# Performance work log

Hardware: AMD Instinct MI355X
Metric: run time of the kernel (lower is better)

The kernel has to match this reference:

```python
import jax, jax.numpy as jnp
import numpy as np
from jax import lax

K = 100
NUM_CLASSES = 80
MIN_X = 1; MIN_Y = 1; MAX_X = 4; MAX_Y = 4   # int(base_layer_range/16) for [16,64,16,64]
KEEP = 300
IOU_TH = 0.5
ROI_H = 2 * MAX_Y + 1  # 9
ROI_W = 2 * MAX_X + 1  # 9
MASK_OUT = 36          # 9 -> two stride-2 deconvs -> 36
SCALE = (36.0 - 1.0) / (9.0 - 1.0)
BN_INV = 1.0 / np.sqrt(1.0 + 1e-3)  # BN eval, running mean 0 / var 1, eps=1e-3
SIZES = [(64, 64), (32, 32), (16, 16)]


def bilinear(img, xx, yy):
    # img [..., H, W]; xx, yy same shape S; border-clamped bilinear sample -> [..., *S]
    H, W = img.shape[-2], img.shape[-1]
    xx = jnp.clip(xx, 0.0, W - 1.0)
    yy = jnp.clip(yy, 0.0, H - 1.0)
    x0f = jnp.floor(xx); y0f = jnp.floor(yy)
    wx = xx - x0f; wy = yy - y0f
    x0 = x0f.astype(jnp.int32); y0 = y0f.astype(jnp.int32)
    x1 = jnp.minimum(x0 + 1, W - 1); y1 = jnp.minimum(y0 + 1, H - 1)
    v00 = img[..., y0, x0]; v01 = img[..., y0, x1]
    v10 = img[..., y1, x0]; v11 = img[..., y1, x1]
    return (1 - wy) * ((1 - wx) * v00 + wx * v01) + wy * ((1 - wx) * v10 + wx * v11)


def roi_align(feat, boxes):
    # feat [C,H,W], boxes [N,4] in feat coords -> [N,C,ROI_H,ROI_W] (sampling_ratio=1)
    n = boxes.shape[0]
    x1, y1, x2, y2 = boxes[:, 0], boxes[:, 1], boxes[:, 2], boxes[:, 3]
    jx = (jnp.arange(ROI_W, dtype=jnp.float32) + 0.5) / ROI_W
    jy = (jnp.arange(ROI_H, dtype=jnp.float32) + 0.5) / ROI_H
    gx = x1[:, None] + (x2 - x1)[:, None] * jx  # [N,ROI_W]
    gy = y1[:, None] + (y2 - y1)[:, None] * jy  # [N,ROI_H]
    xx = jnp.broadcast_to(gx[:, None, :], (n, ROI_H, ROI_W))
    yy = jnp.broadcast_to(gy[:, :, None], (n, ROI_H, ROI_W))
    out = bilinear(feat, xx, yy)  # [C,N,ROI_H,ROI_W]
    return jnp.transpose(out, (1, 0, 2, 3))


def crop_resize(masks, boxes):
    # masks [N,h,w], boxes [N,4] -> [N,MASK_OUT,MASK_OUT]
    n = boxes.shape[0]
    t = jnp.arange(MASK_OUT, dtype=jnp.float32) / (MASK_OUT - 1.0)
    x1, y1, x2, y2 = boxes[:, 0], boxes[:, 1], boxes[:, 2], boxes[:, 3]
    gx = x1[:, None] + (x2 - x1)[:, None] * t
    gy = y1[:, None] + (y2 - y1)[:, None] * t
    xx = jnp.broadcast_to(gx[:, None, :], (n, MASK_OUT, MASK_OUT))
    yy = jnp.broadcast_to(gy[:, :, None], (n, MASK_OUT, MASK_OUT))
    return jax.vmap(bilinear)(masks, xx, yy)


def nms_keep(boxes, scores):
    # greedy NMS, faithful to torchvision semantics; returns bool keep flags [N]
    n = boxes.shape[0]
    x1, y1, x2, y2 = boxes[:, 0], boxes[:, 1], boxes[:, 2], boxes[:, 3]
    area = (x2 - x1) * (y2 - y1)
    ix1 = jnp.maximum(x1[:, None], x1[None, :]); iy1 = jnp.maximum(y1[:, None], y1[None, :])
    ix2 = jnp.minimum(x2[:, None], x2[None, :]); iy2 = jnp.minimum(y2[:, None], y2[None, :])
    inter = jnp.clip(ix2 - ix1, 0.0) * jnp.clip(iy2 - iy1, 0.0)
    iou = inter / (area[:, None] + area[None, :] - inter + 1e-9)
    order = jnp.argsort(-scores)  # stable
    def step(carry, idx):
        supp, keep = carry
        k = jnp.logical_not(supp[idx])
        keep = keep.at[idx].set(k)
        supp = jnp.logical_or(supp, jnp.logical_and(k, iou[idx] > IOU_TH))
        return (supp, keep), None
    init = (jnp.zeros((n,), bool), jnp.zeros((n,), bool))
    (_, keep), _ = lax.scan(step, init, order)
    return keep


def _conv(x, w, b, pad):
    y = lax.conv_general_dilated(x, w, (1, 1), [(pad, pad), (pad, pad)],
                                 dimension_numbers=('NCHW', 'OIHW', 'NCHW'))
    return y + b[None, :, None, None]


def _deconv(x, w, b):
    # ConvTranspose2d(k=2, s=2): fractionally-strided conv, doubles spatial size
    y = lax.conv_general_dilated(x, w, (1, 1), [(1, 1), (1, 1)], lhs_dilation=(2, 2),
                                 dimension_numbers=('NCHW', 'OIHW', 'NCHW'))
    return y + b[None, :, None, None]


def _bn(x, g, b):
    return x * (g * BN_INV)[None, :, None, None] + b[None, :, None, None]


def mask_head(x, c1_w, c1_b, mid_w, mid_b, bn_g, bn_b, d1_w, d1_b, d2_w, d2_b, c5_w, c5_b, c6_w, c6_b):
    r = jax.nn.relu
    h = r(_bn(_conv(x, c1_w, c1_b, 1), bn_g[0], bn_b[0]))
    for j in range(3):  # conv2..conv4
        h = r(_bn(_conv(h, mid_w[j], mid_b[j], 1), bn_g[1 + j], bn_b[1 + j]))
    h = r(_deconv(h, d1_w, d1_b))
    h = r(_bn(_conv(h, c5_w, c5_b, 1), bn_g[4], bn_b[4]))
    h = r(_deconv(h, d2_w, d2_b))
    return jax.nn.sigmoid(_conv(h, c6_w, c6_b, 0))


def _decode_layer(heat, tlr, brr, i, H0, W0):
    C, H, W = heat.shape
    hw = H * W
    scores, inds = lax.top_k(heat.reshape(-1), K)
    clses = (inds // hw).astype(jnp.float32)
    rem = inds % hw
    ys = (rem // W).astype(jnp.float32)
    xs = (rem % W).astype(jnp.float32)
    t = tlr.reshape(2, hw)[:, rem]  # [2,K]
    b = brr.reshape(2, hw)[:, rem]
    rx = float(MAX_X - MIN_X); ry = float(MAX_Y - MIN_Y)
    cx = (MAX_X + MIN_X) / 2.0;  cy = (MAX_Y + MIN_Y) / 2.0
    tlx = jnp.clip(xs - (rx * t[0] + cx), 0.0, float(W))
    tly = jnp.clip(ys - (ry * t[1] + cy), 0.0, float(H))
    brx = jnp.clip(xs + (rx * b[0] + cx), 0.0, float(W))
    bry = jnp.clip(ys + (ry * b[1] + cy), 0.0, float(H))
    boxes = jnp.stack([tlx, tly, brx, bry], 1)
    sc = jnp.where((brx < tlx) | (bry < tly), -1.0, scores)
    mb = jnp.stack([xs - MAX_X, ys - MAX_Y, xs + MAX_X, ys + MAX_Y,
                    jnp.full((K,), float(i))], 1)
    s2, order = lax.top_k(sc, K)  # num_dets(1000) >= K -> full sort by score
    boxes = boxes[order]; mb = mb[order]; cls = clses[order]
    lay = jnp.full((K,), float(i))
    cols = jnp.stack([s2, s2, lay, cls], 1)
    bws = jnp.concatenate([boxes, cols], 1)  # boxes_without_scaling [K,8]
    scale = jnp.array([W0 / W, H0 / H, W0 / W, H0 / H], jnp.float32)
    dets = jnp.concatenate([boxes * scale, cols], 1)
    return dets, bws, mb


def _decode_one(h0, h1, h2, t0, t1, t2, b0, b1, b2, f0, f1, f2,
                c1_w, c1_b, mid_w, mid_b, bn_g, bn_b, d1_w, d1_b, d2_w, d2_b,
                c5_w, c5_b, c6_w, c6_b):
    heats = (h0, h1, h2); tls = (t0, t1, t2); brs = (b0, b1, b2); feats = (f0, f1, f2)
    H0, W0 = heats[0].shape[1], heats[0].shape[2]
    dets_l, bws_l, mb_l = [], [], []
    for i in range(3):
        d, bw, mb = _decode_layer(heats[i], tls[i], brs[i], i, H0, W0)
        dets_l.append(d); bws_l.append(bw); mb_l.append(mb)
    dets = jnp.concatenate(dets_l, 0)   # [300,8]
    bws = jnp.concatenate(bws_l, 0)
    mb = jnp.concatenate(mb_l, 0)       # [300,5]
    # NMS faithful to source: boxes = detections[:,1:5], scores = detections[:,4]
    keep = nms_keep(dets[:, 1:5], dets[:, 4])
    sel = jnp.argsort(-jnp.where(keep, dets[:, 4], -1e9))[:KEEP]
    dets = dets[sel]; bws = bws[sel]; mb = mb[sel]
    # sort by mask layer index descending (features processed last->first)
    ord2 = jnp.argsort(-mb[:, 4])
    dets = dets[ord2]; bws = bws[ord2]; mb = mb[ord2]
    # ROI pool each box from its own layer's feature map
    pooled = jnp.stack([roi_align(feats[i], mb[:, :4]) for i in range(3)], 0)  # [3,N,C,9,9]
    lay = jnp.clip(mb[:, 4].astype(jnp.int32), 0, 2)
    rois = pooled[lay, jnp.arange(KEEP)]  # [N,256,9,9]
    masks_all = mask_head(rois, c1_w, c1_b, mid_w, mid_b, bn_g, bn_b,
                          d1_w, d1_b, d2_w, d2_b, c5_w, c5_b, c6_w, c6_b)  # [N,80,36,36]
    cls = jnp.clip(dets[:, 7].astype(jnp.int32), 0, NUM_CLASSES - 1)
    masks = masks_all[jnp.arange(KEEP), cls]  # [N,36,36] (one-hot scatter/select)
    bws4 = bws[:, :4] - jnp.tile(mb[:, :2], (1, 2))
    norm_boxes = SCALE * bws4
    masks = crop_resize(masks, norm_boxes)
    return dets, masks


def setup_inputs():
    key = jax.random.key(0)
    ks = jax.random.split(key, 32)
    B = 1
    inp = {}
    for i, (H, W) in enumerate(SIZES):
        inp['heat%d' % i] = jax.random.uniform(ks[i], (B, NUM_CLASSES, H, W), jnp.float32)
        inp['tl%d' % i] = 0.1 * jax.random.normal(ks[3 + i], (B, 2, H, W), jnp.float32)
        inp['br%d' % i] = 0.1 * jax.random.normal(ks[6 + i], (B, 2, H, W), jnp.float32)
        inp['feat%d' % i] = jax.random.normal(ks[9 + i], (B, 256, H, W), jnp.float32)
    inp['c1_w'] = 0.05 * jax.random.normal(ks[12], (256, 256, 3, 3), jnp.float32)
    inp['c1_b'] = jnp.zeros((256,), jnp.float32)
    inp['mid_w'] = 0.05 * jax.random.normal(ks[13], (3, 256, 256, 3, 3), jnp.float32)
    inp['mid_b'] = jnp.zeros((3, 256), jnp.float32)
    inp['bn_g'] = jnp.ones((5, 256), jnp.float32)
    inp['bn_b'] = jnp.zeros((5, 256), jnp.float32)
    inp['d1_w'] = 0.05 * jax.random.normal(ks[14], (256, 256, 2, 2), jnp.float32)
    inp['d1_b'] = jnp.zeros((256,), jnp.float32)
    inp['d2_w'] = 0.05 * jax.random.normal(ks[15], (256, 256, 2, 2), jnp.float32)
    inp['d2_b'] = jnp.zeros((256,), jnp.float32)
    inp['c5_w'] = 0.05 * jax.random.normal(ks[16], (256, 256, 3, 3), jnp.float32)
    inp['c5_b'] = jnp.zeros((256,), jnp.float32)
    inp['c6_w'] = 0.05 * jax.random.normal(ks[17], (NUM_CLASSES, 256, 1, 1), jnp.float32)
    inp['c6_b'] = jnp.zeros((NUM_CLASSES,), jnp.float32)
    return inp


def reference(heat0, heat1, heat2, tl0, tl1, tl2, br0, br1, br2, feat0, feat1, feat2,
              c1_w, c1_b, mid_w, mid_b, bn_g, bn_b, d1_w, d1_b, d2_w, d2_b,
              c5_w, c5_b, c6_w, c6_b):
    dets, masks = jax.vmap(_decode_one, in_axes=(0,) * 12 + (None,) * 14)(
        heat0, heat1, heat2, tl0, tl1, tl2, br0, br1, br2, feat0, feat1, feat2,
        c1_w, c1_b, mid_w, mid_b, bn_g, bn_b, d1_w, d1_b, d2_w, d2_b, c5_w, c5_b, c6_w, c6_b)
    return dets, masks  # [B,300,8], [B,300,36,36]
```

## Files before the change

### kernel.cpp

```cpp
#include <hip/hip_runtime.h>
#include <math.h>

typedef __attribute__((ext_vector_type(8))) short bf16x8;
typedef __attribute__((ext_vector_type(4))) float f32x4;

__device__ __forceinline__ unsigned fkey_u(float v){
  unsigned b = __float_as_uint(v);
  return (b & 0x80000000u) ? ~b : (b | 0x80000000u);
}
__device__ __forceinline__ float fkey_inv(unsigned m){
  unsigned b = (m & 0x80000000u) ? (m & 0x7fffffffu) : ~m;
  return __uint_as_float(b);
}
__device__ __forceinline__ unsigned short f2bf(float f){
  unsigned u = __float_as_uint(f);
  unsigned r = (u + 0x7fffu + ((u>>16)&1u)) >> 16;
  return (unsigned short)r;
}
__device__ __forceinline__ unsigned long long shfl_xor_u64(unsigned long long v, int mask){
  int lo = __shfl_xor((int)(unsigned)(v & 0xFFFFFFFFull), mask, 64);
  int hi = __shfl_xor((int)(unsigned)(v >> 32), mask, 64);
  return ((unsigned long long)(unsigned)hi << 32) | (unsigned long long)(unsigned)lo;
}
__device__ __forceinline__ unsigned long long bshfl_u64(unsigned long long v, int lane){
  int lo = __shfl((int)(unsigned)(v & 0xFFFFFFFFull), lane, 64);
  int hi = __shfl((int)(unsigned)(v >> 32), lane, 64);
  return ((unsigned long long)(unsigned)hi << 32) | (unsigned long long)(unsigned)lo;
}
#define BNI 0.9995003746877732f

template<int E, int J>
__device__ __forceinline__ void reg_step(unsigned long long* key, int t, int k2){
  #pragma unroll
  for (int r=0;r<E;r++){
    if ((r & J)==0){
      int e = t*E + r;
      bool desc = ((e & k2)==0);
      unsigned long long a=key[r], b=key[r^J];
      if (desc ? (a<b) : (a>b)){ key[r]=b; key[r^J]=a; }
    }
  }
}
template<int E>
__device__ __forceinline__ void reg_tail(unsigned long long* key, int t, int k2, int jstart){
  if constexpr (E>=8) { if (jstart>=4) reg_step<E,4>(key,t,k2); }
  if constexpr (E>=4) { if (jstart>=2) reg_step<E,2>(key,t,k2); }
  if (jstart>=1) reg_step<E,1>(key,t,k2);
}
template<int E>
__device__ void bitonic_desc(unsigned long long* key, unsigned long long* lds){
  const int t = threadIdx.x;
  const int N = E*256;
  for (int k2=2;k2<=N;k2<<=1){
    for (int j=k2>>1; j>=E; j>>=1){
      int w = j/E;
      bool lower = ((t & w)==0);
      bool desc  = (((t*E) & k2)==0);
      bool keep_max = (desc == lower);
      if (w < 64){
        #pragma unroll
        for (int r=0;r<E;r++){
          unsigned long long mine=key[r];
          unsigned long long o=shfl_xor_u64(mine, w);
          bool gt = mine > o;
          key[r] = keep_max ? (gt?mine:o) : (gt?o:mine);
        }
      } else {
        __syncthreads();
        #pragma unroll
        for (int r=0;r<E;r++) lds[t*E+r]=key[r];
        __syncthreads();
        #pragma unroll
        for (int r=0;r<E;r++){
          unsigned long long mine=key[r];
          unsigned long long o=lds[(t*E+r)^j];
          bool gt = mine > o;
          key[r] = keep_max ? (gt?mine:o) : (gt?o:mine);
        }
      }
    }
    int jstart = ((k2>>1) < (E>>1)) ? (k2>>1) : (E>>1);
    reg_tail<E>(key,t,k2,jstart);
  }
  __syncthreads();
  #pragma unroll
  for (int r=0;r<E;r++) lds[t*E+r]=key[r];
  __syncthreads();
}

__global__ __launch_bounds__(256) void k_sel1(
    const float* __restrict__ h0, const float* __restrict__ h1, const float* __restrict__ h2,
    unsigned long long* __restrict__ c1)
{
  int b = blockIdx.x;
  int layer, chunk;
  if (b < 320){ layer=0; chunk=b; }
  else if (b < 400){ layer=1; chunk=b-320; }
  else { layer=2; chunk=b-400; }
  const float* heat = (layer==0)?h0:((layer==1)?h1:h2);
  __shared__ unsigned long long lds[1024];
  unsigned long long key[4];
  int t = threadIdx.x;
  int base = chunk*1024 + t*4;
  float4 v = *(const float4*)(heat + base);
  key[0] = ((unsigned long long)fkey_u(v.x)<<32) | (unsigned long long)(0xFFFFFFFFu - (unsigned)(base+0));
  key[1] = ((unsigned long long)fkey_u(v.y)<<32) | (unsigned long long)(0xFFFFFFFFu - (unsigned)(base+1));
  key[2] = ((unsigned long long)fkey_u(v.z)<<32) | (unsigned long long)(0xFFFFFFFFu - (unsigned)(base+2));
  key[3] = ((unsigned long long)fkey_u(v.w)<<32) | (unsigned long long)(0xFFFFFFFFu - (unsigned)(base+3));
  bitonic_desc<4>(key, lds);
  if (t<100) c1[(size_t)b*100 + t] = lds[t];
}

__global__ __launch_bounds__(256) void k_sel2(
    const unsigned long long* __restrict__ c1, unsigned long long* __restrict__ c2)
{
  int b = blockIdx.x;
  __shared__ unsigned long long lds[2048];
  unsigned long long key[8];
  int t=threadIdx.x;
  const unsigned long long* src = c1 + (size_t)b*2000;
  #pragma unroll
  for (int r=0;r<8;r++){
    int i=t*8+r;
    key[r] = (i<2000)? src[i] : 0ull;
  }
  bitonic_desc<8>(key, lds);
  if (t<100) c2[(size_t)b*100+t]=lds[t];
}

__global__ __launch_bounds__(256) void k_sel3_decode(
    const unsigned long long* __restrict__ c2,
    const float* __restrict__ tl0,const float* __restrict__ tl1,const float* __restrict__ tl2,
    const float* __restrict__ br0,const float* __restrict__ br1,const float* __restrict__ br2,
    float* __restrict__ dets, float* __restrict__ bws, float* __restrict__ mbw)
{
  int layer = blockIdx.x;
  int hw = 4096 >> (layer*2);
  int W = 64>>layer;
  float Wf = (float)W;
  const float* tl = (layer==0)?tl0:((layer==1)?tl1:tl2);
  const float* br = (layer==0)?br0:((layer==1)?br1:br2);
  int base = (layer==0)?0:((layer==1)?1600:2000);
  int cnt  = (layer==0)?1600:((layer==1)?400:100);
  __shared__ unsigned long long lds[2048];
  __shared__ float scl[100];
  unsigned long long key[8];
  int t = threadIdx.x;
  #pragma unroll
  for (int r=0;r<8;r++){
    int i=t*8+r;
    key[r] = (i<cnt)? c2[base+i] : 0ull;
  }
  bitonic_desc<8>(key, lds);
  unsigned long long kwin=0;
  if (t<100) kwin = lds[t];
  float tlx=0,tly=0,brx=0,bry=0,xs=0,ys=0,clsfv=0,scv=0;
  if (t<100){
    unsigned m=(unsigned)(kwin>>32);
    unsigned gidx = 0xFFFFFFFFu - (unsigned)(kwin & 0xFFFFFFFFull);
    float val = fkey_inv(m);
    int cls = (int)(gidx / (unsigned)hw);
    int rem = (int)(gidx % (unsigned)hw);
    int iy = rem / W, ix = rem % W;
    xs = (float)ix; ys = (float)iy; clsfv = (float)cls;
    float t0=tl[rem], t1=tl[hw+rem], b0=br[rem], b1=br[hw+rem];
    tlx = fminf(fmaxf(xs - (3.0f*t0 + 2.5f), 0.0f), Wf);
    tly = fminf(fmaxf(ys - (3.0f*t1 + 2.5f), 0.0f), Wf);
    brx = fminf(fmaxf(xs + (3.0f*b0 + 2.5f), 0.0f), Wf);
    bry = fminf(fmaxf(ys + (3.0f*b1 + 2.5f), 0.0f), Wf);
    scv = ((brx<tlx)||(bry<tly)) ? -1.0f : val;
    scl[t]=scv;
  }
  __syncthreads();
  if (t<100){
    int rank=0;
    for (int i=0;i<100;i++){
      float si=scl[i];
      rank += ((si>scv)||(si==scv && i<t)) ? 1 : 0;
    }
    int row = layer*100 + rank;
    float sx = (float)(1<<layer);
    float* dr = dets + row*8;
    dr[0]=tlx*sx; dr[1]=tly*sx; dr[2]=brx*sx; dr[3]=bry*sx;
    dr[4]=scv; dr[5]=scv; dr[6]=(float)layer; dr[7]=clsfv;
    float* bwr = bws + row*8;
    bwr[0]=tlx;bwr[1]=tly;bwr[2]=brx;bwr[3]=bry;bwr[4]=scv;bwr[5]=scv;bwr[6]=(float)layer;bwr[7]=clsfv;
    float* mr = mbw + row*5;
    mr[0]=xs-4.0f; mr[1]=ys-4.0f; mr[2]=xs+4.0f; mr[3]=ys+4.0f; mr[4]=(float)layer;
  }
}

#define NMS_STEP(P, OC, M) { \
  int idx=__shfl((OC),(P),64); \
  unsigned long long supw=bshfl_u64(sup, idx>>6); \
  int kq=(int)((~(supw>>(idx&63)))&1ull); \
  if (t==0) keep_[idx]=kq; \
  unsigned long long v0=bshfl_u64(M[0],(P)); \
  unsigned long long v1=bshfl_u64(M[1],(P)); \
  unsigned long long v2=bshfl_u64(M[2],(P)); \
  unsigned long long v3=bshfl_u64(M[3],(P)); \
  unsigned long long v4=bshfl_u64(M[4],(P)); \
  unsigned long long mv=(t==0)?v0:((t==1)?v1:((t==2)?v2:((t==3)?v3:((t==4)?v4:0ull)))); \
  if (kq) sup|=mv; }

__global__ __launch_bounds__(320) void k_nms(
    const float* __restrict__ dets, const float* __restrict__ bws, const float* __restrict__ mbw,
    float* __restrict__ out_dets, float* __restrict__ mbf, int* __restrict__ clsf,
    int* __restrict__ layf, float* __restrict__ nbox)
{
  __shared__ __align__(16) float4 bq[300];
  __shared__ __align__(16) float sc[300];
  __shared__ __align__(16) float kk[300];
  __shared__ __align__(16) float lq[300];
  __shared__ float lyv[300];
  __shared__ unsigned long long sm_ord[300][5];
  __shared__ int order_[300], keep_[300], sel_[300], fperm[300];
  int t = threadIdx.x;
  float X1=0,Y1=0,X2=0,Y2=0,S=0,A=0;
  if (t<300){
    const float* r = dets + t*8;
    X1=r[1];Y1=r[2];X2=r[3];Y2=r[4];
    S=r[4];
    A=(X2-X1)*(Y2-Y1);
    bq[t]=make_float4(X1,Y1,X2,Y2);
    sc[t]=S;
    lyv[t]=mbw[t*5+4];
  }
  __syncthreads();
  if (t<300){
    int rank=0;
    for (int j4=0;j4<75;j4++){
      float4 s4=*(const float4*)&sc[j4*4];
      int j=j4*4;
      rank += ((s4.x>S)||(s4.x==S&&(j+0)<t)) ? 1:0;
      rank += ((s4.y>S)||(s4.y==S&&(j+1)<t)) ? 1:0;
      rank += ((s4.z>S)||(s4.z==S&&(j+2)<t)) ? 1:0;
      rank += ((s4.w>S)||(s4.w==S&&(j+3)<t)) ? 1:0;
    }
    unsigned long long wrow[5];
    #pragma unroll
    for (int jw=0;jw<5;jw++){
      unsigned long long bits=0;
      int lim=(jw==4)?44:64;
      for (int jj=0;jj<lim;jj++){
        int j=jw*64+jj;
        float4 q=bq[j];
        float aj=(q.z-q.x)*(q.w-q.y);
        float ix1=fmaxf(X1,q.x), iy1=fmaxf(Y1,q.y);
        float ix2=fminf(X2,q.z), iy2=fminf(Y2,q.w);
        float it=fmaxf(ix2-ix1,0.f)*fmaxf(iy2-iy1,0.f);
        float iou=it/(A+aj-it+1e-9f);
        bits |= ((unsigned long long)(iou>0.5f))<<jj;
      }
      wrow[jw]=bits;
    }
    order_[rank]=t;
    #pragma unroll
    for (int q=0;q<5;q++) sm_ord[rank][q]=wrow[q];
  }
  __syncthreads();
  if (t<64){
    int o0=order_[t], o1=order_[64+t], o2=order_[128+t], o3=order_[192+t];
    int o4=(t<44)? order_[256+t] : 0;
    unsigned long long m0[5],m1[5],m2[5],m3[5],m4[5];
    #pragma unroll
    for (int q=0;q<5;q++){
      m0[q]=sm_ord[t][q]; m1[q]=sm_ord[64+t][q];
      m2[q]=sm_ord[128+t][q]; m3[q]=sm_ord[192+t][q];
      m4[q]=(t<44)? sm_ord[256+t][q] : 0ull;
    }
    unsigned long long sup=0;
    for (int p=0;p<64;p++) NMS_STEP(p,o0,m0);
    for (int p=0;p<64;p++) NMS_STEP(p,o1,m1);
    for (int p=0;p<64;p++) NMS_STEP(p,o2,m2);
    for (int p=0;p<64;p++) NMS_STEP(p,o3,m3);
    for (int p=0;p<44;p++) NMS_STEP(p,o4,m4);
  }
  __syncthreads();
  if (t<300) kk[t] = keep_[t] ? sc[t] : -1000000000.0f;
  __syncthreads();
  float KV=0; int rank2=0;
  if (t<300){
    KV=kk[t];
    for (int j4=0;j4<75;j4++){
      float4 s4=*(const float4*)&kk[j4*4];
      int j=j4*4;
      rank2 += ((s4.x>KV)||(s4.x==KV&&(j+0)<t)) ? 1:0;
      rank2 += ((s4.y>KV)||(s4.y==KV&&(j+1)<t)) ? 1:0;
      rank2 += ((s4.z>KV)||(s4.z==KV&&(j+2)<t)) ? 1:0;
      rank2 += ((s4.w>KV)||(s4.w==KV&&(j+3)<t)) ? 1:0;
    }
    sel_[rank2]=t;
  }
  __syncthreads();
  if (t<300) lq[t]=lyv[sel_[t]];
  __syncthreads();
  if (t<300){
    float L=lq[t]; int rank3=0;
    for (int j4=0;j4<75;j4++){
      float4 s4=*(const float4*)&lq[j4*4];
      int j=j4*4;
      rank3 += ((s4.x>L)||(s4.x==L&&(j+0)<t)) ? 1:0;
      rank3 += ((s4.y>L)||(s4.y==L&&(j+1)<t)) ? 1:0;
      rank3 += ((s4.z>L)||(s4.z==L&&(j+2)<t)) ? 1:0;
      rank3 += ((s4.w>L)||(s4.w==L&&(j+3)<t)) ? 1:0;
    }
    fperm[rank3]=sel_[t];
  }
  __syncthreads();
  if (t<300){
    int src=fperm[t];
    const float* dr=dets+src*8;
    #pragma unroll
    for (int c=0;c<8;c++) out_dets[t*8+c]=dr[c];
    const float* mr=mbw+src*5;
    #pragma unroll
    for (int c=0;c<5;c++) mbf[t*5+c]=mr[c];
    int cc=(int)dr[7]; cc = cc<0?0:(cc>79?79:cc); clsf[t]=cc;
    int lv=(int)mr[4]; lv = lv<0?0:(lv>2?2:lv); layf[t]=lv;
    const float* bw=bws+src*8;
    nbox[t*4+0]=4.375f*(bw[0]-mr[0]);
    nbox[t*4+1]=4.375f*(bw[1]-mr[1]);
    nbox[t*4+2]=4.375f*(bw[2]-mr[0]);
    nbox[t*4+3]=4.375f*(bw[3]-mr[1]);
  }
}

__global__ __launch_bounds__(256) void k_roi(
    const float* __restrict__ f0,const float* __restrict__ f1,const float* __restrict__ f2,
    const float* __restrict__ mbf, const int* __restrict__ layf,
    unsigned short* __restrict__ rois, int r0)
{
  int nl = blockIdx.x; int g = r0 + nl;
  __shared__ int ix0[9], ix1[9], iy0[9], iy1[9];
  __shared__ float wx[9], wy[9];
  int lay = layf[g];
  int W = 64>>lay;
  float Wf1 = (float)(W-1);
  const float* feat = (lay==0)?f0:((lay==1)?f1:f2);
  int t=threadIdx.x;
  if (t<9){
    float x1=mbf[g*5+0], x2=mbf[g*5+2];
    float jx = ((float)t + 0.5f)/9.0f;
    float gx = x1 + (x2-x1)*jx;
    float xx = fminf(fmaxf(gx,0.0f), Wf1);
    float x0f = floorf(xx);
    wx[t]=xx-x0f;
    int x0=(int)x0f; ix0[t]=x0; ix1[t]=min(x0+1,W-1);
  } else if (t>=16 && t<25){
    int j=t-16;
    float y1=mbf[g*5+1], y2=mbf[g*5+3];
    float jy=((float)j+0.5f)/9.0f;
    float gy=y1+(y2-y1)*jy;
    float yy=fminf(fmaxf(gy,0.0f),Wf1);
    float y0f=floorf(yy);
    wy[j]=yy-y0f;
    int y0=(int)y0f; iy0[j]=y0; iy1[j]=min(y0+1,W-1);
  }
  __syncthreads();
  int c=t;
  const float* fp = feat + (size_t)c*W*W;
  unsigned short* op = rois + (size_t)nl*81*256;
  for (int p=0;p<81;p++){
    int py=p/9, px=p%9;
    float v00=fp[iy0[py]*W+ix0[px]];
    float v01=fp[iy0[py]*W+ix1[px]];
    float v10=fp[iy1[py]*W+ix0[px]];
    float v11=fp[iy1[py]*W+ix1[px]];
    float wxx=wx[px], wyy=wy[py];
    float v = (1.0f-wyy)*((1.0f-wxx)*v00 + wxx*v01) + wyy*((1.0f-wxx)*v10 + wxx*v11);
    op[(size_t)p*256 + c] = f2bf(v);
  }
}

__global__ __launch_bounds__(64) void k_wprep3(
    const float* __restrict__ c1w, const float* __restrict__ midw, const float* __restrict__ c5w,
    unsigned short* __restrict__ WB)
{
  int b = blockIdx.x, c = blockIdx.y, l = threadIdx.x;
  int t = b>>7;
  const float* src = (c==0)? c1w : (c<=3 ? midw + (size_t)(c-1)*589824 : c5w);
  unsigned short* dst = WB + (size_t)c*589824 + ((size_t)b<<9) + l*8;
  int co = (b&15)*16 + (l&15);
  int cib = ((b>>4)&7)*32 + ((l>>4)<<3);
  #pragma unroll
  for (int j=0;j<8;j++) dst[j] = f2bf(src[((size_t)co*256 + cib + j)*9 + t]);
}
__global__ __launch_bounds__(64) void k_wprep2(
    const float* __restrict__ d1w, const float* __restrict__ d2w,
    unsigned short* __restrict__ WD)
{
  int b = blockIdx.x, c = blockIdx.y, l = threadIdx.x;
  int t = b>>7;
  const float* src = (c==0)? d1w : d2w;
  unsigned short* dst = WD + (size_t)c*262144 + ((size_t)b<<9) + l*8;
  int co = (b&15)*16 + (l&15);
  int cib = ((b>>4)&7)*32 + ((l>>4)<<3);
  #pragma unroll
  for (int j=0;j<8;j++) dst[j] = f2bf(src[((size_t)co*256 + cib + j)*4 + t]);
}

__global__ __launch_bounds__(256,3) void k_mconv9h(
    const unsigned short* __restrict__ Xg, unsigned short* __restrict__ Yg,
    const unsigned short* __restrict__ WBc,
    const float* __restrict__ Bc, const float* __restrict__ Gg, const float* __restrict__ Bn)
{
  __shared__ __align__(16) unsigned short Xp[88*264];
  int tid=threadIdx.x, l=tid&63, w=tid>>6;
  int h=blockIdx.y;
  int rlo = h ? 4 : -1;
  const unsigned short* Xr = Xg + (size_t)blockIdx.x*81*256;
  for (int idx=tid; idx<88*32; idx+=256){
    int pp=idx>>5, k8=idx&31;
    int y=pp/11 + rlo, x=pp%11 - 1;
    uint4 v{0,0,0,0};
    if ((unsigned)y<9u && (unsigned)x<9u) v = *(const uint4*)(Xr + ((y*9+x)<<8) + (k8<<3));
    *(uint4*)&Xp[pp*264 + (k8<<3)] = v;
  }
  __syncthreads();
  int mbase = h*48;
  int pixb[3];
  #pragma unroll
  for (int mt=0;mt<3;mt++){
    int m=mbase+mt*16+(l&15); if(m>80)m=80;
    pixb[mt]=(m/9 - rlo)*11 + (m%9) + 1;
  }
  int kg=(l>>4)<<3;
  f32x4 acc[3][4] = {};
  const unsigned short* wbase = WBc + (size_t)l*8;
  for (int t9=0;t9<9;t9++){
    int toff=(t9/3-1)*11 + (t9%3-1);
    for (int kc=0;kc<8;kc++){
      bf16x8 a[3], b[4];
      #pragma unroll
      for (int mt=0;mt<3;mt++) a[mt] = *(const bf16x8*)&Xp[(pixb[mt]+toff)*264 + (kc<<5) + kg];
      #pragma unroll
      for (int nn=0;nn<4;nn++) b[nn] = *(const bf16x8*)(wbase + ((size_t)(((t9<<3)+kc)*16 + (w<<2)+nn)<<9));
      #pragma unroll
      for (int mt=0;mt<3;mt++){
        #pragma unroll
        for (int nn=0;nn<4;nn++)
          acc[mt][nn] = __builtin_amdgcn_mfma_f32_16x16x32_bf16(a[mt], b[nn], acc[mt][nn], 0,0,0);
      }
    }
  }
  unsigned short* Yr = Yg + (size_t)blockIdx.x*81*256;
  int rb=(l>>4)<<2;
  #pragma unroll
  for (int nn=0;nn<4;nn++){
    int co=(w<<6)+(nn<<4)+(l&15);
    float bc=Bc[co], gm=Gg[co]*BNI, bb=Bn[co];
    #pragma unroll
    for (int mt=0;mt<3;mt++){
      #pragma unroll
      for (int r=0;r<4;r++){
        int m=mbase+mt*16+rb+r;
        if (m<81 || h==0){
          if (m<81){
            float v=fmaxf((acc[mt][nn][r]+bc)*gm+bb, 0.f);
            Yr[m*256+co]=f2bf(v);
          }
        }
      }
    }
  }
}

__global__ __launch_bounds__(256,2) void k_mdeconv1(
    const unsigned short* __restrict__ Xg, unsigned short* __restrict__ Yg,
    const unsigned short* __restrict__ WD1, const float* __restrict__ Bd)
{
  __shared__ __align__(16) unsigned short Xp[81*264];
  int tid=threadIdx.x, l=tid&63, w=tid>>6;
  int tp=blockIdx.y;
  const unsigned short* Xr = Xg + (size_t)blockIdx.x*81*256;
  for (int idx=tid; idx<81*32; idx+=256){
    int pp=idx>>5, k8=idx&31;
    *(uint4*)&Xp[pp*264+(k8<<3)] = *(const uint4*)(Xr + (pp<<8)+(k8<<3));
  }
  __syncthreads();
  int pixb[6];
  #pragma unroll
  for (int mt=0;mt<6;mt++){ int m=mt*16+(l&15); pixb[mt]=(m>80)?80:m; }
  int kg=(l>>4)<<3;
  f32x4 acc[6][4] = {};
  const unsigned short* wbase = WD1 + (size_t)tp*65536 + (size_t)l*8;
  for (int kc=0;kc<8;kc++){
    bf16x8 a[6], b[4];
    #pragma unroll
    for (int mt=0;mt<6;mt++) a[mt] = *(const bf16x8*)&Xp[pixb[mt]*264 + (kc<<5) + kg];
    #pragma unroll
    for (int nn=0;nn<4;nn++) b[nn] = *(const bf16x8*)(wbase + ((size_t)(kc*16 + (w<<2)+nn)<<9));
    #pragma unroll
    for (int mt=0;mt<6;mt++){
      #pragma unroll
      for (int nn=0;nn<4;nn++)
        acc[mt][nn] = __builtin_amdgcn_mfma_f32_16x16x32_bf16(a[mt], b[nn], acc[mt][nn], 0,0,0);
    }
  }
  unsigned short* Yr = Yg + (size_t)blockIdx.x*324*256;
  int ky=tp>>1, kx=tp&1;
  int rb=(l>>4)<<2;
  #pragma unroll
  for (int nn=0;nn<4;nn++){
    int co=(w<<6)+(nn<<4)+(l&15);
    float bd=Bd[co];
    #pragma unroll
    for (int mt=0;mt<6;mt++){
      #pragma unroll
      for (int r=0;r<4;r++){
        int m=mt*16+rb+r;
        if (m<81){
          int iy=m/9, ix=m%9;
          int opx=(2*iy+1-ky)*18 + (2*ix+1-kx);
          Yr[opx*256+co]=f2bf(fmaxf(acc[mt][nn][r]+bd,0.f));
        }
      }
    }
  }
}

__global__ __launch_bounds__(256,2) void k_mconv18(
    const unsigned short* __restrict__ Xg, unsigned short* __restrict__ Yg,
    const unsigned short* __restrict__ WBc,
    const float* __restrict__ Bc, const float* __restrict__ Gg, const float* __restrict__ Bn)
{
  __shared__ __align__(16) unsigned short Xp[160*136];
  int tid=threadIdx.x, l=tid&63, w=tid>>6;
  int rg=blockIdx.y, ch=blockIdx.z;
  const unsigned short* Xr = Xg + (size_t)blockIdx.x*324*256;
  int pixb[7];
  #pragma unroll
  for (int mt=0;mt<7;mt++){ int m=mt*16+(l&15); if(m>107)m=107; pixb[mt]=(m/18)*20+(m%18); }
  int kg=(l>>4)<<3;
  f32x4 acc[7][2] = {};
  const unsigned short* wbase = WBc + (size_t)l*8;
  for (int h=0;h<2;h++){
    __syncthreads();
    for (int idx=tid; idx<160*16; idx+=256){
      int pp=idx>>4, k8=idx&15;
      int py=rg*6-1+pp/20, px=pp%20-1;
      uint4 v{0,0,0,0};
      if ((unsigned)py<18u && (unsigned)px<18u)
        v = *(const uint4*)(Xr + ((py*18+px)<<8) + (h<<7) + (k8<<3));
      *(uint4*)&Xp[pp*136 + (k8<<3)] = v;
    }
    __syncthreads();
    for (int t9=0;t9<9;t9++){
      int toff=(t9/3)*20 + (t9%3);
      for (int kc=0;kc<4;kc++){
        int kcg=(h<<2)+kc;
        bf16x8 a[7], b[2];
        #pragma unroll
        for (int mt=0;mt<7;mt++) a[mt] = *(const bf16x8*)&Xp[(pixb[mt]+toff)*136 + (kc<<5) + kg];
        #pragma unroll
        for (int nn=0;nn<2;nn++) b[nn] = *(const bf16x8*)(wbase + ((size_t)(((t9<<3)+kcg)*16 + (ch<<3)+(w<<1)+nn)<<9));
        #pragma unroll
        for (int mt=0;mt<7;mt++){
          #pragma unroll
          for (int nn=0;nn<2;nn++)
            acc[mt][nn] = __builtin_amdgcn_mfma_f32_16x16x32_bf16(a[mt], b[nn], acc[mt][nn], 0,0,0);
        }
      }
    }
  }
  unsigned short* Yr = Yg + (size_t)blockIdx.x*324*256;
  int rb=(l>>4)<<2;
  #pragma unroll
  for (int nn=0;nn<2;nn++){
    int co=(ch<<7)+(w<<5)+(nn<<4)+(l&15);
    float bc=Bc[co], gm=Gg[co]*BNI, bb=Bn[co];
    #pragma unroll
    for (int mt=0;mt<7;mt++){
      #pragma unroll
      for (int r=0;r<4;r++){
        int m=mt*16+rb+r;
        if (m<108){
          int opx=rg*108+m;
          Yr[opx*256+co]=f2bf(fmaxf((acc[mt][nn][r]+bc)*gm+bb, 0.f));
        }
      }
    }
  }
}

__global__ __launch_bounds__(256,2) void k_mdec2c6(
    const unsigned short* __restrict__ Xg,
    const unsigned short* __restrict__ WD2, const float* __restrict__ Bd,
    const float* __restrict__ W6, const float* __restrict__ B6,
    const int* __restrict__ clsf, float* __restrict__ mask36, int r0)
{
  __shared__ __align__(16) unsigned short Xp[108*264];
  __shared__ float part[4][112];
  int tid=threadIdx.x, l=tid&63, w=tid>>6;
  int tp=blockIdx.y, rg=blockIdx.z;
  int g=r0+blockIdx.x;
  const unsigned short* Xr = Xg + (size_t)blockIdx.x*324*256 + (size_t)rg*108*256;
  for (int idx=tid; idx<108*32; idx+=256){
    int pp=idx>>5, k8=idx&31;
    *(uint4*)&Xp[pp*264+(k8<<3)] = *(const uint4*)(Xr + (pp<<8)+(k8<<3));
  }
  __syncthreads();
  int pixb[7];
  #pragma unroll
  for (int mt=0;mt<7;mt++){ int m=mt*16+(l&15); pixb[mt]=(m>107)?107:m; }
  int kg=(l>>4)<<3;
  f32x4 acc[7][4] = {};
  const unsigned short* wbase = WD2 + (size_t)tp*65536 + (size_t)l*8;
  for (int kc=0;kc<8;kc++){
    bf16x8 a[7], b[4];
    #pragma unroll
    for (int mt=0;mt<7;mt++) a[mt] = *(const bf16x8*)&Xp[pixb[mt]*264 + (kc<<5) + kg];
    #pragma unroll
    for (int nn=0;nn<4;nn++) b[nn] = *(const bf16x8*)(wbase + ((size_t)(kc*16 + (w<<2)+nn)<<9));
    #pragma unroll
    for (int mt=0;mt<7;mt++){
      #pragma unroll
      for (int nn=0;nn<4;nn++)
        acc[mt][nn] = __builtin_amdgcn_mfma_f32_16x16x32_bf16(a[mt], b[nn], acc[mt][nn], 0,0,0);
    }
  }
  int cls=clsf[g];
  float w6v[4], bdv[4];
  #pragma unroll
  for (int nn=0;nn<4;nn++){
    int co=(w<<6)+(nn<<4)+(l&15);
    w6v[nn]=W6[(size_t)cls*256+co];
    bdv[nn]=Bd[co];
  }
  int rb=(l>>4)<<2;
  #pragma unroll
  for (int mt=0;mt<7;mt++){
    float s0=0.f,s1=0.f,s2=0.f,s3=0.f;
    #pragma unroll
    for (int nn=0;nn<4;nn++){
      s0 += fmaxf(acc[mt][nn][0]+bdv[nn],0.f)*w6v[nn];
      s1 += fmaxf(acc[mt][nn][1]+bdv[nn],0.f)*w6v[nn];
      s2 += fmaxf(acc[mt][nn][2]+bdv[nn],0.f)*w6v[nn];
      s3 += fmaxf(acc[mt][nn][3]+bdv[nn],0.f)*w6v[nn];
    }
    #pragma unroll
    for (int o=1;o<16;o<<=1){
      s0 += __shfl_xor(s0,o,64);
      s1 += __shfl_xor(s1,o,64);
      s2 += __shfl_xor(s2,o,64);
      s3 += __shfl_xor(s3,o,64);
    }
    if ((l&15)==0){
      int mb=mt*16+rb;
      part[w][mb+0]=s0; part[w][mb+1]=s1; part[w][mb+2]=s2; part[w][mb+3]=s3;
    }
  }
  __syncthreads();
  if (tid<108){
    float lg = part[0][tid]+part[1][tid]+part[2][tid]+part[3][tid] + B6[cls];
    int pg=rg*108+tid, iy=pg/18, ix=pg%18;
    int ky=tp>>1, kx=tp&1;
    mask36[(size_t)g*1296 + (2*iy+1-ky)*36 + (2*ix+1-kx)] = 1.0f/(1.0f+expf(-lg));
  }
}

__global__ __launch_bounds__(256) void k_crop(
    const float* __restrict__ mask36, const float* __restrict__ nbox,
    float* __restrict__ outm)
{
  int r=blockIdx.x;
  __shared__ float m[1296];
  int t=threadIdx.x;
  for (int i=t;i<1296;i+=256) m[i]=mask36[(size_t)r*1296+i];
  float x1=nbox[r*4+0], y1=nbox[r*4+1], x2=nbox[r*4+2], y2=nbox[r*4+3];
  __syncthreads();
  for (int p=t;p<1296;p+=256){
    int oy=p/36, ox=p%36;
    float tx=(float)ox/35.0f, ty=(float)oy/35.0f;
    float gx=x1+(x2-x1)*tx, gy=y1+(y2-y1)*ty;
    float xx=fminf(fmaxf(gx,0.f),35.0f), yy=fminf(fmaxf(gy,0.f),35.0f);
    float x0f=floorf(xx), y0f=floorf(yy);
    float wxv=xx-x0f, wyv=yy-y0f;
    int x0=(int)x0f, y0=(int)y0f;
    int x1i=min(x0+1,35), y1i=min(y0+1,35);
    float v00=m[y0*36+x0], v01=m[y0*36+x1i], v10=m[y1i*36+x0], v11=m[y1i*36+x1i];
    outm[(size_t)r*1296+p]=(1.f-wyv)*((1.f-wxv)*v00+wxv*v01)+wyv*((1.f-wxv)*v10+wxv*v11);
  }
}

extern "C" void kernel_launch(void* const* d_in, const int* in_sizes, int n_in,
                              void* d_out, int out_size, void* d_ws, size_t ws_size,
                              hipStream_t stream) {
  int iH[3], iT[3], iB[3], iF[3];
  if (n_in >= 12 && in_sizes[1] == 2*64*64) {
    for (int l=0;l<3;l++){ iH[l]=l*4+0; iT[l]=l*4+1; iB[l]=l*4+2; iF[l]=l*4+3; }
  } else {
    for (int l=0;l<3;l++){ iH[l]=l; iT[l]=3+l; iB[l]=6+l; iF[l]=9+l; }
  }
  const float* heat0=(const float*)d_in[iH[0]];
  const float* heat1=(const float*)d_in[iH[1]];
  const float* heat2=(const float*)d_in[iH[2]];
  const float* tl0=(const float*)d_in[iT[0]];
  const float* tl1=(const float*)d_in[iT[1]];
  const float* tl2=(const float*)d_in[iT[2]];
  const float* br0=(const float*)d_in[iB[0]];
  const float* br1=(const float*)d_in[iB[1]];
  const float* br2=(const float*)d_in[iB[2]];
  const float* feat0=(const float*)d_in[iF[0]];
  const float* feat1=(const float*)d_in[iF[1]];
  const float* feat2=(const float*)d_in[iF[2]];
  const float* c1w=(const float*)d_in[12];
  const float* c1b=(const float*)d_in[13];
  const float* midw=(const float*)d_in[14];
  const float* midb=(const float*)d_in[15];
  const float* bng=(const float*)d_in[16];
  const float* bnb=(const float*)d_in[17];
  const float* d1w=(const float*)d_in[18];
  const float* d1b=(const float*)d_in[19];
  const float* d2w=(const float*)d_in[20];
  const float* d2b=(const float*)d_in[21];
  const float* c5w=(const float*)d_in[22];
  const float* c5b=(const float*)d_in[23];
  const float* c6w=(const float*)d_in[24];
  const float* c6b=(const float*)d_in[25];
  float* out=(float*)d_out;

  char* ws=(char*)d_ws;
  size_t cur=0;
  auto alloc=[&](size_t bytes)->char*{
    char* p=ws+cur;
    cur=(cur+bytes+255)&~(size_t)255;
    return p;
  };
  unsigned short* WB=(unsigned short*)alloc(5ull*589824*2);
  unsigned short* WD=(unsigned short*)alloc(2ull*262144*2);
  unsigned long long* c1s=(unsigned long long*)alloc(420ull*100*8);
  unsigned long long* c2s=(unsigned long long*)alloc(21ull*100*8);
  float* detsw=(float*)alloc(300*8*4);
  float* bwsw=(float*)alloc(300*8*4);
  float* mbw=(float*)alloc(300*5*4);
  float* mbf=(float*)alloc(300*5*4);
  int* clsf=(int*)alloc(300*4);
  int* layf=(int*)alloc(300*4);
  float* nbox=(float*)alloc(300*4*4);
  float* mask36=(float*)alloc(300ull*1296*4);
  size_t fixed=cur;
  size_t perroi = (size_t)(2*81 + 2*324)*256*2;
  size_t avail = (ws_size>fixed+4096)? (ws_size-fixed-4096):0;
  int NRC = (int)(avail/perroi);
  if (NRC>300) NRC=300;
  if (NRC<1) NRC=1;
  unsigned short* X0 =(unsigned short*)alloc((size_t)NRC*81*256*2);
  unsigned short* B9 =(unsigned short*)alloc((size_t)NRC*81*256*2);
  unsigned short* C18=(unsigned short*)alloc((size_t)NRC*324*256*2);
  unsigned short* D18=(unsigned short*)alloc((size_t)NRC*324*256*2);

  k_wprep3<<<dim3(1152,5),dim3(64),0,stream>>>(c1w,midw,c5w,WB);
  k_wprep2<<<dim3(512,2),dim3(64),0,stream>>>(d1w,d2w,WD);

  k_sel1<<<dim3(420),dim3(256),0,stream>>>(heat0,heat1,heat2,c1s);
  k_sel2<<<dim3(21),dim3(256),0,stream>>>(c1s,c2s);
  k_sel3_decode<<<dim3(3),dim3(256),0,stream>>>(c2s,tl0,tl1,tl2,br0,br1,br2,detsw,bwsw,mbw);
  k_nms<<<dim3(1),dim3(320),0,stream>>>(detsw,bwsw,mbw,out,mbf,clsf,layf,nbox);

  for (int r0=0;r0<300;r0+=NRC){
    int nr = (300-r0 < NRC)? (300-r0) : NRC;
    k_roi<<<dim3(nr),dim3(256),0,stream>>>(feat0,feat1,feat2,mbf,layf,X0,r0);
    k_mconv9h<<<dim3(nr,2),dim3(256),0,stream>>>(X0,B9,WB,               c1b,       bng,      bnb);
    k_mconv9h<<<dim3(nr,2),dim3(256),0,stream>>>(B9,X0,WB+1ull*589824,   midb,      bng+256,  bnb+256);
    k_mconv9h<<<dim3(nr,2),dim3(256),0,stream>>>(X0,B9,WB+2ull*589824,   midb+256,  bng+512,  bnb+512);
    k_mconv9h<<<dim3(nr,2),dim3(256),0,stream>>>(B9,X0,WB+3ull*589824,   midb+512,  bng+768,  bnb+768);
    k_mdeconv1<<<dim3(nr,4),dim3(256),0,stream>>>(X0,C18,WD,d1b);
    k_mconv18<<<dim3(nr,3,2),dim3(256),0,stream>>>(C18,D18,WB+4ull*589824, c5b, bng+1024, bnb+1024);
    k_mdec2c6<<<dim3(nr,4,3),dim3(256),0,stream>>>(D18,WD+262144,d2b,c6w,c6b,clsf,mask36,r0);
  }
  k_crop<<<dim3(300),dim3(256),0,stream>>>(mask36,nbox,out+2400);
}
```

Measured before the change: 696.2 us.

## Serialize NMS scan on one thread over score-sorted boxes; raise conv occupancy

The NMS kernel now sorts boxes by score first, builds the IoU bitmask rows in that sorted order, and runs the greedy suppression scan on a single thread with masked ORs. This replaces the old 64-lane shuffle-heavy loop that issued several 64-bit broadcasts per step. Keep flags are mapped back to the original indices through a permutation array. Separately, the mdeconv1 and mconv18 kernels raise their launch-bounds occupancy hint from 2 to 3, which may cause register spills, and a redundant nested condition in the conv epilogue is removed.

```diff
diff --git a/kernel.cpp b/kernel.cpp
--- a/kernel.cpp
+++ b/kernel.cpp
@@ -20,11 +20,6 @@
 __device__ __forceinline__ unsigned long long shfl_xor_u64(unsigned long long v, int mask){
   int lo = __shfl_xor((int)(unsigned)(v & 0xFFFFFFFFull), mask, 64);
   int hi = __shfl_xor((int)(unsigned)(v >> 32), mask, 64);
-  return ((unsigned long long)(unsigned)hi << 32) | (unsigned long long)(unsigned)lo;
-}
-__device__ __forceinline__ unsigned long long bshfl_u64(unsigned long long v, int lane){
-  int lo = __shfl((int)(unsigned)(v & 0xFFFFFFFFull), lane, 64);
-  int hi = __shfl((int)(unsigned)(v >> 32), lane, 64);
   return ((unsigned long long)(unsigned)hi << 32) | (unsigned long long)(unsigned)lo;
 }
 #define BNI 0.9995003746877732f
@@ -190,39 +185,38 @@
   }
 }
 
-#define NMS_STEP(P, OC, M) { \
-  int idx=__shfl((OC),(P),64); \
-  unsigned long long supw=bshfl_u64(sup, idx>>6); \
-  int kq=(int)((~(supw>>(idx&63)))&1ull); \
-  if (t==0) keep_[idx]=kq; \
-  unsigned long long v0=bshfl_u64(M[0],(P)); \
-  unsigned long long v1=bshfl_u64(M[1],(P)); \
-  unsigned long long v2=bshfl_u64(M[2],(P)); \
-  unsigned long long v3=bshfl_u64(M[3],(P)); \
-  unsigned long long v4=bshfl_u64(M[4],(P)); \
-  unsigned long long mv=(t==0)?v0:((t==1)?v1:((t==2)?v2:((t==3)?v3:((t==4)?v4:0ull)))); \
-  if (kq) sup|=mv; }
+#define SCAN_GROUP(SW, BASE, CNT) \
+  _Pragma("unroll 4") \
+  for (int rr=0; rr<CNT; rr++){ \
+    int r = BASE+rr; \
+    unsigned long long w0=sm[r][0],w1=sm[r][1],w2=sm[r][2],w3=sm[r][3],w4=sm[r][4]; \
+    unsigned long long kq = (~(SW>>rr))&1ull; \
+    keepr[r]=(unsigned char)kq; \
+    unsigned long long msk = 0ull - kq; \
+    s0|=w0&msk; s1|=w1&msk; s2|=w2&msk; s3|=w3&msk; s4|=w4&msk; \
+  }
 
 __global__ __launch_bounds__(320) void k_nms(
     const float* __restrict__ dets, const float* __restrict__ bws, const float* __restrict__ mbw,
     float* __restrict__ out_dets, float* __restrict__ mbf, int* __restrict__ clsf,
     int* __restrict__ layf, float* __restrict__ nbox)
 {
-  __shared__ __align__(16) float4 bq[300];
+  __shared__ __align__(16) float4 rb[300];
+  __shared__ float rs[300];
+  __shared__ int orig[300];
   __shared__ __align__(16) float sc[300];
   __shared__ __align__(16) float kk[300];
   __shared__ __align__(16) float lq[300];
   __shared__ float lyv[300];
-  __shared__ unsigned long long sm_ord[300][5];
-  __shared__ int order_[300], keep_[300], sel_[300], fperm[300];
+  __shared__ unsigned long long sm[300][5];
+  __shared__ unsigned char keepr[304];
+  __shared__ int sel_[300], fperm[300];
   int t = threadIdx.x;
-  float X1=0,Y1=0,X2=0,Y2=0,S=0,A=0;
+  float X1=0,Y1=0,X2=0,Y2=0,S=0;
   if (t<300){
     const float* r = dets + t*8;
     X1=r[1];Y1=r[2];X2=r[3];Y2=r[4];
     S=r[4];
-    A=(X2-X1)*(Y2-Y1);
-    bq[t]=make_float4(X1,Y1,X2,Y2);
     sc[t]=S;
     lyv[t]=mbw[t*5+4];
   }
@@ -237,47 +231,42 @@
       rank += ((s4.z>S)||(s4.z==S&&(j+2)<t)) ? 1:0;
       rank += ((s4.w>S)||(s4.w==S&&(j+3)<t)) ? 1:0;
     }
-    unsigned long long wrow[5];
+    rb[rank]=make_float4(X1,Y1,X2,Y2);
+    rs[rank]=S;
+    orig[rank]=t;
+  }
+  __syncthreads();
+  if (t<300){
+    float4 me=rb[t];
+    float A=(me.z-me.x)*(me.w-me.y);
     #pragma unroll
     for (int jw=0;jw<5;jw++){
       unsigned long long bits=0;
       int lim=(jw==4)?44:64;
       for (int jj=0;jj<lim;jj++){
         int j=jw*64+jj;
-        float4 q=bq[j];
+        float4 q=rb[j];
         float aj=(q.z-q.x)*(q.w-q.y);
-        float ix1=fmaxf(X1,q.x), iy1=fmaxf(Y1,q.y);
-        float ix2=fminf(X2,q.z), iy2=fminf(Y2,q.w);
+        float ix1=fmaxf(me.x,q.x), iy1=fmaxf(me.y,q.y);
+        float ix2=fminf(me.z,q.z), iy2=fminf(me.w,q.w);
         float it=fmaxf(ix2-ix1,0.f)*fmaxf(iy2-iy1,0.f);
         float iou=it/(A+aj-it+1e-9f);
         bits |= ((unsigned long long)(iou>0.5f))<<jj;
       }
-      wrow[jw]=bits;
-    }
-    order_[rank]=t;
-    #pragma unroll
-    for (int q=0;q<5;q++) sm_ord[rank][q]=wrow[q];
-  }
-  __syncthreads();
-  if (t<64){
-    int o0=order_[t], o1=order_[64+t], o2=order_[128+t], o3=order_[192+t];
-    int o4=(t<44)? order_[256+t] : 0;
-    unsigned long long m0[5],m1[5],m2[5],m3[5],m4[5];
-    #pragma unroll
-    for (int q=0;q<5;q++){
-      m0[q]=sm_ord[t][q]; m1[q]=sm_ord[64+t][q];
-      m2[q]=sm_ord[128+t][q]; m3[q]=sm_ord[192+t][q];
-      m4[q]=(t<44)? sm_ord[256+t][q] : 0ull;
-    }
-    unsigned long long sup=0;
-    for (int p=0;p<64;p++) NMS_STEP(p,o0,m0);
-    for (int p=0;p<64;p++) NMS_STEP(p,o1,m1);
-    for (int p=0;p<64;p++) NMS_STEP(p,o2,m2);
-    for (int p=0;p<64;p++) NMS_STEP(p,o3,m3);
-    for (int p=0;p<44;p++) NMS_STEP(p,o4,m4);
-  }
-  __syncthreads();
-  if (t<300) kk[t] = keep_[t] ? sc[t] : -1000000000.0f;
+      sm[t][jw]=bits;
+    }
+  }
+  __syncthreads();
+  if (t==0){
+    unsigned long long s0=0,s1=0,s2=0,s3=0,s4=0;
+    SCAN_GROUP(s0,0,64)
+    SCAN_GROUP(s1,64,64)
+    SCAN_GROUP(s2,128,64)
+    SCAN_GROUP(s3,192,64)
+    SCAN_GROUP(s4,256,44)
+  }
+  __syncthreads();
+  if (t<300) kk[orig[t]] = keepr[t] ? rs[t] : -1000000000.0f;
   __syncthreads();
   float KV=0; int rank2=0;
   if (t<300){
@@ -455,18 +444,16 @@
       #pragma unroll
       for (int r=0;r<4;r++){
         int m=mbase+mt*16+rb+r;
-        if (m<81 || h==0){
-          if (m<81){
-            float v=fmaxf((acc[mt][nn][r]+bc)*gm+bb, 0.f);
-            Yr[m*256+co]=f2bf(v);
-          }
+        if (m<81){
+          float v=fmaxf((acc[mt][nn][r]+bc)*gm+bb, 0.f);
+          Yr[m*256+co]=f2bf(v);
         }
       }
     }
   }
 }
 
-__global__ __launch_bounds__(256,2) void k_mdeconv1(
+__global__ __launch_bounds__(256,3) void k_mdeconv1(
     const unsigned short* __restrict__ Xg, unsigned short* __restrict__ Yg,
     const unsigned short* __restrict__ WD1, const float* __restrict__ Bd)
 {
@@ -520,7 +507,7 @@
   }
 }
 
-__global__ __launch_bounds__(256,2) void k_mconv18(
+__global__ __launch_bounds__(256,3) void k_mconv18(
     const unsigned short* __restrict__ Xg, unsigned short* __restrict__ Yg,
     const unsigned short* __restrict__ WBc,
     const float* __restrict__ Bc, const float* __restrict__ Gg, const float* __restrict__ Bn)
```

Measured after the change: 657.0 us. 1.06x faster.
